# Kernel optimization log

Hardware: AMD Instinct MI355X
Metric: run time of the kernel (lower is better)

The kernel has to match this reference:

```python
import jax, jax.numpy as jnp
import numpy as np
from jax import lax

B_, L, D, EXPAND, N, R, K = 2, 1024, 1024, 2, 16, 64, 4
ED = EXPAND * D


def setup_inputs() -> dict:
    key = jax.random.key(0)
    ks = jax.random.split(key, 8)
    x = jax.random.normal(ks[0], (B_, L, D), dtype=jnp.float32)
    in_proj_w = jax.random.normal(ks[1], (2 * ED, D), dtype=jnp.float32) * (D ** -0.5)
    in_proj_b = jnp.zeros((2 * ED,), jnp.float32)
    conv_w = jax.random.normal(ks[2], (ED, 1, K), dtype=jnp.float32) * (K ** -0.5)
    conv_b = jnp.zeros((ED,), jnp.float32)
    x_proj_w = jax.random.normal(ks[3], (R + 2 * N, ED), dtype=jnp.float32) * (ED ** -0.5)
    dt_proj_w = jax.random.uniform(ks[4], (ED, R), jnp.float32, -(R ** -0.5), R ** -0.5)
    # inverse-softplus of dt ~ U[log(dt_min), log(dt_max)] (matches torch init)
    dt = jnp.exp(jax.random.uniform(ks[5], (ED,), jnp.float32) * (np.log(0.1) - np.log(0.001)) + np.log(0.001))
    dt_proj_b = dt + jnp.log(-jnp.expm1(-dt))  # softplus^{-1}(dt)
    A_log = jnp.log(jnp.broadcast_to(jnp.arange(1, N + 1, dtype=jnp.float32), (ED, N)))
    D_param = jnp.ones((ED,), jnp.float32)
    out_proj_w = jax.random.normal(ks[6], (D, ED), dtype=jnp.float32) * (ED ** -0.5)
    return {"x": x, "in_proj_w": in_proj_w, "in_proj_b": in_proj_b, "conv_w": conv_w,
            "conv_b": conv_b, "x_proj_w": x_proj_w, "dt_proj_w": dt_proj_w,
            "dt_proj_b": dt_proj_b, "A_log": A_log, "D_param": D_param,
            "out_proj_w": out_proj_w}


def _mamba_fwd(x, in_proj_w, in_proj_b, conv_w, conv_b, x_proj_w, dt_proj_w,
               dt_proj_b, A_log, D_param, out_proj_w):
    xz = x @ in_proj_w.T + in_proj_b                       # (B, L, 2*ED)
    xc, z = jnp.split(xz, 2, axis=-1)                      # (B, L, ED) each
    # causal depthwise conv over time (pad left K-1, valid)
    xc = xc.transpose(0, 2, 1)                             # (B, ED, L)
    xc = lax.conv_general_dilated(xc, conv_w, window_strides=(1,),
                                  padding=[(K - 1, 0)], feature_group_count=ED)
    xc = xc + conv_b[None, :, None]
    xc = jax.nn.silu(xc.transpose(0, 2, 1))                # (B, L, ED)
    # SSM params
    A = -jnp.exp(A_log)                                    # (ED, N)
    dbc = xc @ x_proj_w.T                                  # (B, L, R+2N)
    dt, Bmat, Cmat = jnp.split(dbc, [R, R + N], axis=-1)
    dt = jax.nn.softplus(dt @ dt_proj_w.T + dt_proj_b)     # (B, L, ED)
    dA = jnp.exp(dt[..., None] * A)                        # (B, L, ED, N)
    dBx = (dt * xc)[..., None] * Bmat[:, :, None, :]       # (B, L, ED, N)
    # parallel scan: h_t = dA_t * h_{t-1} + dBx_t
    def combine(e1, e2):
        a1, b1 = e1
        a2, b2 = e2
        return a1 * a2, a2 * b1 + b2
    _, hs = lax.associative_scan(combine, (dA, dBx), axis=1)  # (B, L, ED, N)
    y = jnp.einsum('bln,blen->ble', Cmat, hs) + D_param * xc  # (B, L, ED)
    out = (y * jax.nn.silu(z)) @ out_proj_w.T                 # (B, L, D)
    return out


def reference(x, in_proj_w, in_proj_b, conv_w, conv_b, x_proj_w, dt_proj_w,
              dt_proj_b, A_log, D_param, out_proj_w):
    return _mamba_fwd(x, in_proj_w, in_proj_b, conv_w, conv_b, x_proj_w,
                      dt_proj_w, dt_proj_b, A_log, D_param, out_proj_w)
```

## Files before the change

### kernel.cpp

```cpp
#include <hip/hip_runtime.h>
#include <cstddef>


#define BL   2048
#define DIM  1024
#define ED   2048
#define NST  16
#define RLOW 64
#define CH   64
#define LC   16
#define SK   16
#define DBCN 196608

typedef __attribute__((ext_vector_type(4))) float   f32x4;
typedef __attribute__((ext_vector_type(8))) __bf16  bf16x8;
typedef __attribute__((ext_vector_type(8))) unsigned short us8;

__device__ __forceinline__ float silu_(float x) {
  return x / (1.f + __expf(-x));
}

__device__ __forceinline__ float softplus_(float x) {
  const float v = __logf(1.f + __expf(x));
  return (x > 20.f) ? x : v;
}

__device__ __forceinline__ unsigned short f2b(float x) {
  union { float f; unsigned int u; } v; v.f = x;
  unsigned int r = v.u + 0x7FFFu + ((v.u >> 16) & 1u);
  return (unsigned short)(r >> 16);
}

__device__ __forceinline__ float b2f(unsigned short u) {
  union { unsigned int i; float f; } v; v.i = (unsigned int)u << 16; return v.f;
}

__device__ __forceinline__ f32x4 mfma_bf16(us8 a, us8 b, f32x4 c) {
  return __builtin_amdgcn_mfma_f32_16x16x32_bf16(
      __builtin_bit_cast(bf16x8, a), __builtin_bit_cast(bf16x8, b), c, 0, 0, 0);
}

template <int N> __device__ __forceinline__ void vwaitN() {
  if constexpr (N == 0)      asm volatile("s_waitcnt vmcnt(0)" ::: "memory");
  else if constexpr (N == 3) asm volatile("s_waitcnt vmcnt(3)" ::: "memory");
  else if constexpr (N == 4) asm volatile("s_waitcnt vmcnt(4)" ::: "memory");
  else if constexpr (N == 6) asm volatile("s_waitcnt vmcnt(6)" ::: "memory");
  else if constexpr (N == 8) asm volatile("s_waitcnt vmcnt(8)" ::: "memory");
}

#define GLOAD_LDS16(gaddr, laddr)                                              \
  __builtin_amdgcn_global_load_lds(                                            \
      (const __attribute__((address_space(1))) unsigned int*)(gaddr),          \
      (__attribute__((address_space(3))) unsigned int*)(laddr), 16, 0, 0)

template <int BM, int BN, int ACT, bool OBF, int SWZ>
__global__ __launch_bounds__(256) void gemm_bf16(
    const unsigned short* __restrict__ A,
    const unsigned short* __restrict__ W,
    const float* __restrict__ bias,
    void* __restrict__ Cp, int ldc, int Nout, int Kloop, int lda, int sstride)
{
  constexpr int BK     = 32;
  constexpr int FM     = BM / 32;
  constexpr int FN     = BN / 32;
  constexpr int NLA    = BM / 64;
  constexpr int NLW    = BN / 64;
  constexpr int VPS    = NLA + NLW;
  constexpr int ABYTES = BM * BK * 2;
  constexpr int WBYTES = BN * BK * 2;
  __shared__ char smem[4 * (ABYTES + WBYTES)];

  const int tid  = threadIdx.x;
  const int w    = tid >> 6;
  const int lane = tid & 63;
  const int wr   = w >> 1, wc = w & 1;

  int bx = blockIdx.x, by = blockIdx.y;
  if (SWZ) {
    const int nwg  = gridDim.x * gridDim.y;
    const int flat = by * gridDim.x + bx;
    const int nid  = (flat & 7) * (nwg >> 3) + (flat >> 3);
    bx = nid % gridDim.x;
    by = nid / gridDim.x;
  }
  const int bm   = bx * BM;
  const int bn   = by * BN;
  const int kb   = blockIdx.z * Kloop;

  f32x4 acc[FM][FN];
#pragma unroll
  for (int m = 0; m < FM; ++m)
#pragma unroll
    for (int n = 0; n < FN; ++n) acc[m][n] = (f32x4){0.f, 0.f, 0.f, 0.f};

  const int srow = (w << 4) | (lane & 15);
  const int kch  = lane >> 4;
  const int wofs = w * 1024;

  const unsigned short* Ag = A + (size_t)(bm + srow) * lda + kb + kch * 8;
  const unsigned short* Wg = W + (size_t)(bn + srow) * lda + kb + kch * 8;

#define STAGE(cur, k0)                                                         \
  {                                                                            \
    char* ab = smem + (cur) * (ABYTES + WBYTES);                               \
    char* wb = ab + ABYTES;                                                    \
    _Pragma("unroll")                                                          \
    for (int j = 0; j < NLA; ++j)                                              \
      GLOAD_LDS16(Ag + (size_t)(j * 64) * lda + (k0), ab + j * 4096 + wofs);   \
    _Pragma("unroll")                                                          \
    for (int j = 0; j < NLW; ++j)                                              \
      GLOAD_LDS16(Wg + (size_t)(j * 64) * lda + (k0), wb + j * 4096 + wofs);   \
  }

  const int NT = Kloop / BK;
  STAGE(0, 0);
  if (NT > 1) STAGE(1, BK);
  if (NT > 2) STAGE(2, 2 * BK);

  for (int t = 0; t < NT; ++t) {
    if (t <= NT - 3)      vwaitN<2 * VPS>();
    else if (t == NT - 2) vwaitN<VPS>();
    else                  vwaitN<0>();
    __builtin_amdgcn_sched_barrier(0);
    __builtin_amdgcn_s_barrier();
    __builtin_amdgcn_sched_barrier(0);
    if (t + 3 < NT) STAGE((t + 3) & 3, (size_t)(t + 3) * BK);

    const char* ab = smem + (t & 3) * (ABYTES + WBYTES);
    const char* wb = ab + ABYTES;
    us8 af[FM], wf[FN];
#pragma unroll
    for (int m = 0; m < FM; ++m)
      af[m] = *(const us8*)(ab + (wr * FM + m) * 1024 + lane * 16);
#pragma unroll
    for (int n = 0; n < FN; ++n)
      wf[n] = *(const us8*)(wb + (wc * FN + n) * 1024 + lane * 16);
#pragma unroll
    for (int m = 0; m < FM; ++m)
#pragma unroll
      for (int n = 0; n < FN; ++n)
        acc[m][n] = mfma_bf16(af[m], wf[n], acc[m][n]);
  }
#undef STAGE

  const int rbase = (lane >> 4) * 4;
  float* Cf = (float*)Cp + (size_t)blockIdx.z * sstride;
#pragma unroll
  for (int m = 0; m < FM; ++m) {
#pragma unroll
    for (int n = 0; n < FN; ++n) {
      const int col = bn + wc * (BN / 2) + n * 16 + (lane & 15);
      if (col < Nout) {
        const float bv = bias ? bias[col] : 0.f;
#pragma unroll
        for (int r = 0; r < 4; ++r) {
          const int row = bm + wr * (BM / 2) + m * 16 + rbase + r;
          float v = acc[m][n][r] + bv;
          if (ACT == 1) v = softplus_(v);
          if (OBF) ((unsigned short*)Cp)[(size_t)row * ldc + col] = f2b(v);
          else     Cf[(size_t)row * ldc + col] = v;
        }
      }
    }
  }
}

__global__ __launch_bounds__(256) void reduce_dbc_k(
    const float* __restrict__ par, float* __restrict__ dbc,
    unsigned short* __restrict__ dtA)
{
  const int i = blockIdx.x * 256 + threadIdx.x;
  float4 s = ((const float4*)par)[i];
#pragma unroll
  for (int sk = 1; sk < SK; ++sk) {
    float4 v = ((const float4*)(par + (size_t)sk * DBCN))[i];
    s.x += v.x; s.y += v.y; s.z += v.z; s.w += v.w;
  }
  ((float4*)dbc)[i] = s;
  const int row = i / 24, c4 = i % 24;
  if (c4 < 16) {
    ushort4 o;
    o.x = f2b(s.x); o.y = f2b(s.y); o.z = f2b(s.z); o.w = f2b(s.w);
    ((ushort4*)(dtA + (size_t)row * 64))[c4] = o;
  }
}

__global__ __launch_bounds__(256) void reduce_out_k(
    const float* __restrict__ par, float* __restrict__ out)
{
  const int i = blockIdx.x * 256 + threadIdx.x;
  float4 a = ((const float4*)par)[i];
#pragma unroll
  for (int k = 1; k < 4; ++k) {
    float4 b = ((const float4*)(par + (size_t)k * 2097152))[i];
    a.x += b.x; a.y += b.y; a.z += b.z; a.w += b.w;
  }
  ((float4*)out)[i] = a;
}

__global__ __launch_bounds__(256) void cvt_all_k(
    const float* __restrict__ x, const float* __restrict__ inw,
    const float* __restrict__ ow, const float* __restrict__ xpw,
    const float* __restrict__ dtw,
    unsigned short* __restrict__ xb, unsigned short* __restrict__ iwb,
    unsigned short* __restrict__ owb, unsigned short* __restrict__ xpwb,
    unsigned short* __restrict__ dtwb)
{
  const int i = blockIdx.x * 256 + threadIdx.x;
  const float* src; unsigned short* dst; int j;
  if (i < 524288)       { src = x;   dst = xb;  j = i; }
  else if (i < 1572864) { src = inw; dst = iwb; j = i - 524288; }
  else if (i < 2097152) { src = ow;  dst = owb; j = i - 1572864; }
  else if (i < 2162688) {
    j = i - 2097152;
    const int idx = j * 4;
    ushort4 o = {0, 0, 0, 0};
    if ((idx >> 11) < 96) {
      float4 v = *(const float4*)(xpw + idx);
      o.x = f2b(v.x); o.y = f2b(v.y); o.z = f2b(v.z); o.w = f2b(v.w);
    }
    *(ushort4*)(xpwb + idx) = o;
    return;
  } else                { src = dtw; dst = dtwb; j = i - 2162688; }
  float4 v = ((const float4*)src)[j];
  ushort4 o;
  o.x = f2b(v.x); o.y = f2b(v.y); o.z = f2b(v.z); o.w = f2b(v.w);
  ((ushort4*)dst)[j] = o;
}

__global__ __launch_bounds__(256) void conv_silu_k(
    const unsigned short* __restrict__ xzb, const float* __restrict__ cw,
    const float* __restrict__ cb, unsigned short* __restrict__ xcb)
{
  const int idx = blockIdx.x * 256 + threadIdx.x;
  const int row = idx >> 9;
  const int e   = (idx & 511) * 4;
  const int l   = row & 1023;
  const unsigned short* base = xzb + (size_t)(row - l) * (2 * ED) + e;

  float4 cbv = *(const float4*)(cb + e);
  float a0 = cbv.x, a1 = cbv.y, a2 = cbv.z, a3 = cbv.w;
#pragma unroll
  for (int k = 0; k < 4; ++k) {
    const int ls = l - 3 + k;
    if (ls >= 0) {
      ushort4 u = *(const ushort4*)(base + (size_t)ls * (2 * ED));
      a0 += cw[(size_t)(e + 0) * 4 + k] * b2f(u.x);
      a1 += cw[(size_t)(e + 1) * 4 + k] * b2f(u.y);
      a2 += cw[(size_t)(e + 2) * 4 + k] * b2f(u.z);
      a3 += cw[(size_t)(e + 3) * 4 + k] * b2f(u.w);
    }
  }
  ushort4 o;
  o.x = f2b(silu_(a0)); o.y = f2b(silu_(a1));
  o.z = f2b(silu_(a2)); o.w = f2b(silu_(a3));
  *(ushort4*)(xcb + (size_t)row * ED + e) = o;
}

__global__ __launch_bounds__(256, 4) void scan_phase1(
    const unsigned short* __restrict__ dt, const unsigned short* __restrict__ xcb,
    const float* __restrict__ dbc, const float* __restrict__ A_log,
    float* __restrict__ aprod_o, float* __restrict__ bfin_o)
{
  const int g  = blockIdx.x * 256 + threadIdx.x;
  const int e  = g & (ED - 1);
  const int bc = g >> 11;
  const int b  = bc >> 6;
  const int c  = bc & (CH - 1);
  const size_t rowbase = (size_t)b * 1024 + (size_t)c * LC;

  __shared__ float4 sB[LC][4];
  if (threadIdx.x < LC * 4) {
    const int row = threadIdx.x >> 2, q = threadIdx.x & 3;
    sB[row][q] = ((const float4*)(dbc + (rowbase + row) * 96 + RLOW))[q];
  }
  __syncthreads();

  float Aen[NST];
  {
    const float4* Ap = (const float4*)(A_log + (size_t)e * NST);
#pragma unroll
    for (int q = 0; q < 4; ++q) {
      float4 v = Ap[q];
      Aen[q*4+0] = -__expf(v.x); Aen[q*4+1] = -__expf(v.y);
      Aen[q*4+2] = -__expf(v.z); Aen[q*4+3] = -__expf(v.w);
    }
  }

  float dtv[LC], dxv[LC];
#pragma unroll
  for (int i = 0; i < LC; ++i) dtv[i] = b2f(dt[(rowbase + i) * ED + e]);
#pragma unroll
  for (int i = 0; i < LC; ++i)
    dxv[i] = dtv[i] * b2f(xcb[(rowbase + i) * ED + e]);

  float h[NST], ap[NST];
#pragma unroll
  for (int n = 0; n < NST; ++n) { h[n] = 0.f; ap[n] = 1.f; }

  for (int i = 0; i < LC; ++i) {
    float Bv[NST];
#pragma unroll
    for (int q = 0; q < 4; ++q) {
      float4 v = sB[i][q];
      Bv[q*4+0]=v.x; Bv[q*4+1]=v.y; Bv[q*4+2]=v.z; Bv[q*4+3]=v.w;
    }
#pragma unroll
    for (int n = 0; n < NST; ++n) {
      const float dA = __expf(dtv[i] * Aen[n]);
      ap[n] *= dA;
      h[n] = fmaf(dA, h[n], dxv[i] * Bv[n]);
    }
  }

  const size_t obase = ((size_t)(b * ED + e) * CH + c) * NST;
  float4* ao = (float4*)(aprod_o + obase);
  float4* bo = (float4*)(bfin_o + obase);
#pragma unroll
  for (int q = 0; q < 4; ++q) {
    ao[q] = make_float4(ap[q*4+0], ap[q*4+1], ap[q*4+2], ap[q*4+3]);
    bo[q] = make_float4(h[q*4+0],  h[q*4+1],  h[q*4+2],  h[q*4+3]);
  }
}

__global__ __launch_bounds__(256) void scan_phase2(
    const float* __restrict__ aprod, float* __restrict__ bfin)
{
  const int be   = blockIdx.x * 4 + (threadIdx.x >> 6);
  const int lane = threadIdx.x & 63;
  const size_t base = (size_t)be * CH * NST;

  float Aa[NST], Bb[NST];
  {
    const float4* ap4 = (const float4*)(aprod + base);
    const float4* bp4 = (const float4*)(bfin + base);
#pragma unroll
    for (int q = 0; q < 4; ++q) {
      float4 v = ap4[lane * 4 + q];
      Aa[q*4+0]=v.x; Aa[q*4+1]=v.y; Aa[q*4+2]=v.z; Aa[q*4+3]=v.w;
      float4 w = bp4[lane * 4 + q];
      Bb[q*4+0]=w.x; Bb[q*4+1]=w.y; Bb[q*4+2]=w.z; Bb[q*4+3]=w.w;
    }
  }

#pragma unroll
  for (int d = 1; d < 64; d <<= 1) {
#pragma unroll
    for (int r = 0; r < NST; ++r) {
      const float aP = __shfl_up(Aa[r], d);
      const float bP = __shfl_up(Bb[r], d);
      if (lane >= d) {
        Bb[r] = fmaf(Aa[r], bP, Bb[r]);
        Aa[r] *= aP;
      }
    }
  }

#pragma unroll
  for (int r = 0; r < NST; ++r) {
    const float hs = __shfl_up(Bb[r], 1);
    Bb[r] = (lane == 0) ? 0.f : hs;
  }

  float4* ob4 = (float4*)(bfin + base);
#pragma unroll
  for (int q = 0; q < 4; ++q)
    ob4[lane * 4 + q] = make_float4(Bb[q*4+0], Bb[q*4+1], Bb[q*4+2], Bb[q*4+3]);
}

__global__ __launch_bounds__(256, 4) void scan_phase3(
    const unsigned short* __restrict__ dt, const unsigned short* __restrict__ xcb,
    const float* __restrict__ dbc, const float* __restrict__ A_log,
    const float* __restrict__ Dp, const unsigned short* __restrict__ xzb,
    const float* __restrict__ hst, unsigned short* __restrict__ ygb)
{
  const int g  = blockIdx.x * 256 + threadIdx.x;
  const int e  = g & (ED - 1);
  const int bc = g >> 11;
  const int b  = bc >> 6;
  const int c  = bc & (CH - 1);
  const size_t rowbase = (size_t)b * 1024 + (size_t)c * LC;

  __shared__ float4 sBC[LC][8];
  if (threadIdx.x < LC * 8) {
    const int row = threadIdx.x >> 3, q = threadIdx.x & 7;
    sBC[row][q] = ((const float4*)(dbc + (rowbase + row) * 96 + RLOW))[q];
  }
  __syncthreads();

  float Aen[NST];
  {
    const float4* Ap = (const float4*)(A_log + (size_t)e * NST);
#pragma unroll
    for (int q = 0; q < 4; ++q) {
      float4 v = Ap[q];
      Aen[q*4+0] = -__expf(v.x); Aen[q*4+1] = -__expf(v.y);
      Aen[q*4+2] = -__expf(v.z); Aen[q*4+3] = -__expf(v.w);
    }
  }

  float dtv[LC], xcv[LC];
#pragma unroll
  for (int i = 0; i < LC; ++i) dtv[i] = b2f(dt[(rowbase + i) * ED + e]);
#pragma unroll
  for (int i = 0; i < LC; ++i) xcv[i] = b2f(xcb[(rowbase + i) * ED + e]);

  float h[NST];
  {
    const float4* Hp = (const float4*)(hst + ((size_t)(b * ED + e) * CH + c) * NST);
#pragma unroll
    for (int q = 0; q < 4; ++q) {
      float4 v = Hp[q];
      h[q*4+0]=v.x; h[q*4+1]=v.y; h[q*4+2]=v.z; h[q*4+3]=v.w;
    }
  }

  const float De = Dp[e];
  for (int i = 0; i < LC; ++i) {
    const size_t rr = rowbase + i;
    float Bv[NST], Cv[NST];
#pragma unroll
    for (int q = 0; q < 4; ++q) {
      float4 v = sBC[i][q];
      Bv[q*4+0]=v.x; Bv[q*4+1]=v.y; Bv[q*4+2]=v.z; Bv[q*4+3]=v.w;
      float4 w = sBC[i][q + 4];
      Cv[q*4+0]=w.x; Cv[q*4+1]=w.y; Cv[q*4+2]=w.z; Cv[q*4+3]=w.w;
    }
    const float dx = dtv[i] * xcv[i];
    float y = 0.f;
#pragma unroll
    for (int n = 0; n < NST; ++n) {
      const float dA = __expf(dtv[i] * Aen[n]);
      h[n] = fmaf(dA, h[n], dx * Bv[n]);
      y = fmaf(Cv[n], h[n], y);
    }
    y = fmaf(De, xcv[i], y);
    const float zf = b2f(xzb[rr * (2 * ED) + ED + e]);
    ygb[rr * ED + e] = f2b(y * silu_(zf));
  }
}

extern "C" void kernel_launch(void* const* d_in, const int* in_sizes, int n_in,
                              void* d_out, int out_size, void* d_ws, size_t ws_size,
                              hipStream_t stream) {
  const float* x         = (const float*)d_in[0];
  const float* in_w      = (const float*)d_in[1];
  const float* in_b      = (const float*)d_in[2];
  const float* conv_w    = (const float*)d_in[3];
  const float* conv_b    = (const float*)d_in[4];
  const float* xproj_w   = (const float*)d_in[5];
  const float* dtproj_w  = (const float*)d_in[6];
  const float* dtproj_b  = (const float*)d_in[7];
  const float* A_log     = (const float*)d_in[8];
  const float* D_param   = (const float*)d_in[9];
  const float* outproj_w = (const float*)d_in[10];
  float* out = (float*)d_out;

  float* ws    = (float*)d_ws;
  float* dbc   = ws;
  unsigned short* dtbu = (unsigned short*)(dbc + 196608);
  float* aprod = (float*)(dtbu + 4194304);
  float* bfin  = aprod + 4194304;
  float* parx  = bfin  + 4194304;
  unsigned short* xzb  = (unsigned short*)(parx + 3145728);
  unsigned short* xb   = xzb  + 8388608;
  unsigned short* iwb  = xb   + 2097152;
  unsigned short* owb  = iwb  + 4194304;
  unsigned short* xpwb = owb  + 2097152;
  unsigned short* xcb  = xpwb + 262144;
  unsigned short* ygb  = xcb  + 4194304;
  unsigned short* dtA  = ygb  + 4194304;
  unsigned short* dtwb = dtA  + 131072;
  float* paro  = aprod;

  const dim3 blk(256);

  cvt_all_k<<<dim3(2195456 / 256), blk, 0, stream>>>(
      x, in_w, outproj_w, xproj_w, dtproj_w, xb, iwb, owb, xpwb, dtwb);

  gemm_bf16<128, 128, 0, true, 1><<<dim3(BL / 128, 4096 / 128), blk, 0, stream>>>(
      xb, iwb, in_b, xzb, 2 * ED, 2 * ED, DIM, DIM, 0);

  conv_silu_k<<<dim3((BL * (ED / 4)) / 256), blk, 0, stream>>>(
      xzb, conv_w, conv_b, xcb);

  gemm_bf16<128, 128, 0, false, 0><<<dim3(BL / 128, 1, SK), blk, 0, stream>>>(
      xcb, xpwb, nullptr, parx, 96, 96, ED / SK, ED, DBCN);
  reduce_dbc_k<<<dim3(DBCN / 4 / 256), blk, 0, stream>>>(parx, dbc, dtA);

  gemm_bf16<64, 128, 1, true, 0><<<dim3(BL / 64, ED / 128), blk, 0, stream>>>(
      dtA, dtwb, dtproj_b, dtbu, ED, ED, RLOW, RLOW, 0);

  scan_phase1<<<dim3((2 * CH * ED) / 256), blk, 0, stream>>>(
      dtbu, xcb, dbc, A_log, aprod, bfin);
  scan_phase2<<<dim3((2 * ED) / 4), blk, 0, stream>>>(aprod, bfin);
  scan_phase3<<<dim3((2 * CH * ED) / 256), blk, 0, stream>>>(
      dtbu, xcb, dbc, A_log, D_param, xzb, bfin, ygb);

  gemm_bf16<128, 128, 0, false, 0><<<dim3(BL / 128, 1024 / 128, 4), blk, 0, stream>>>(
      ygb, owb, nullptr, paro, DIM, DIM, ED / 4, ED, 2097152);
  reduce_out_k<<<dim3(2097152 / 4 / 256), blk, 0, stream>>>(paro, out);
}
```

Baseline: 191.7 us.

## Give each wave private LDS double buffers and drop block barriers in GEMM

The bf16 GEMM now has each wave load its own A and W sub-tiles into a private double-buffered LDS region instead of sharing a four-stage block-wide buffer. This removes the per-iteration s_barrier, since no wave reads data loaded by another wave. The cost is duplicated global loads, because waves sharing a row or column of the tile each fetch the same data. Prefetch depth also drops from three stages to one, which may expose more memory latency.

```diff
diff --git a/kernel.cpp b/kernel.cpp
--- a/kernel.cpp
+++ b/kernel.cpp
@@ -42,8 +42,6 @@
 
 template <int N> __device__ __forceinline__ void vwaitN() {
   if constexpr (N == 0)      asm volatile("s_waitcnt vmcnt(0)" ::: "memory");
-  else if constexpr (N == 3) asm volatile("s_waitcnt vmcnt(3)" ::: "memory");
-  else if constexpr (N == 4) asm volatile("s_waitcnt vmcnt(4)" ::: "memory");
   else if constexpr (N == 6) asm volatile("s_waitcnt vmcnt(6)" ::: "memory");
   else if constexpr (N == 8) asm volatile("s_waitcnt vmcnt(8)" ::: "memory");
 }
@@ -60,15 +58,14 @@
     const float* __restrict__ bias,
     void* __restrict__ Cp, int ldc, int Nout, int Kloop, int lda, int sstride)
 {
-  constexpr int BK     = 32;
-  constexpr int FM     = BM / 32;
-  constexpr int FN     = BN / 32;
-  constexpr int NLA    = BM / 64;
-  constexpr int NLW    = BN / 64;
-  constexpr int VPS    = NLA + NLW;
-  constexpr int ABYTES = BM * BK * 2;
-  constexpr int WBYTES = BN * BK * 2;
-  __shared__ char smem[4 * (ABYTES + WBYTES)];
+  constexpr int BK  = 32;
+  constexpr int WM  = BM / 2, WN = BN / 2;
+  constexpr int FMW = WM / 16, FNW = WN / 16;
+  constexpr int VPS = FMW + FNW;
+  constexpr int AB  = WM * BK * 2;
+  constexpr int WBb = WN * BK * 2;
+  constexpr int BUF = AB + WBb;
+  __shared__ char smem[4 * 2 * BUF];
 
   const int tid  = threadIdx.x;
   const int w    = tid >> 6;
@@ -83,62 +80,58 @@
     bx = nid % gridDim.x;
     by = nid / gridDim.x;
   }
-  const int bm   = bx * BM;
-  const int bn   = by * BN;
-  const int kb   = blockIdx.z * Kloop;
-
-  f32x4 acc[FM][FN];
-#pragma unroll
-  for (int m = 0; m < FM; ++m)
-#pragma unroll
-    for (int n = 0; n < FN; ++n) acc[m][n] = (f32x4){0.f, 0.f, 0.f, 0.f};
-
-  const int srow = (w << 4) | (lane & 15);
-  const int kch  = lane >> 4;
-  const int wofs = w * 1024;
-
-  const unsigned short* Ag = A + (size_t)(bm + srow) * lda + kb + kch * 8;
-  const unsigned short* Wg = W + (size_t)(bn + srow) * lda + kb + kch * 8;
-
-#define STAGE(cur, k0)                                                         \
+  const int bm = bx * BM;
+  const int bn = by * BN;
+  const int kb = blockIdx.z * Kloop;
+
+  f32x4 acc[FMW][FNW];
+#pragma unroll
+  for (int m = 0; m < FMW; ++m)
+#pragma unroll
+    for (int n = 0; n < FNW; ++n) acc[m][n] = (f32x4){0.f, 0.f, 0.f, 0.f};
+
+  char* wbase = smem + w * 2 * BUF;
+  const unsigned short* Ag =
+      A + (size_t)(bm + wr * WM + (lane & 15)) * lda + kb + (lane >> 4) * 8;
+  const unsigned short* Wg =
+      W + (size_t)(bn + wc * WN + (lane & 15)) * lda + kb + (lane >> 4) * 8;
+
+#define STAGE(bb, k0)                                                          \
   {                                                                            \
-    char* ab = smem + (cur) * (ABYTES + WBYTES);                               \
-    char* wb = ab + ABYTES;                                                    \
+    char* dst = wbase + (bb) * BUF;                                            \
     _Pragma("unroll")                                                          \
-    for (int j = 0; j < NLA; ++j)                                              \
-      GLOAD_LDS16(Ag + (size_t)(j * 64) * lda + (k0), ab + j * 4096 + wofs);   \
+    for (int j = 0; j < FMW; ++j)                                              \
+      GLOAD_LDS16(Ag + (size_t)(j * 16) * lda + (k0), dst + j * 1024);         \
     _Pragma("unroll")                                                          \
-    for (int j = 0; j < NLW; ++j)                                              \
-      GLOAD_LDS16(Wg + (size_t)(j * 64) * lda + (k0), wb + j * 4096 + wofs);   \
+    for (int j = 0; j < FNW; ++j)                                              \
+      GLOAD_LDS16(Wg + (size_t)(j * 16) * lda + (k0), dst + AB + j * 1024);    \
   }
 
   const int NT = Kloop / BK;
   STAGE(0, 0);
   if (NT > 1) STAGE(1, BK);
-  if (NT > 2) STAGE(2, 2 * BK);
 
   for (int t = 0; t < NT; ++t) {
-    if (t <= NT - 3)      vwaitN<2 * VPS>();
-    else if (t == NT - 2) vwaitN<VPS>();
-    else                  vwaitN<0>();
+    if (t + 1 < NT) vwaitN<VPS>();
+    else            vwaitN<0>();
     __builtin_amdgcn_sched_barrier(0);
-    __builtin_amdgcn_s_barrier();
+
+    const char* bufc = wbase + (t & 1) * BUF;
+    us8 af[FMW], wf[FNW];
+#pragma unroll
+    for (int m = 0; m < FMW; ++m)
+      af[m] = *(const us8*)(bufc + m * 1024 + lane * 16);
+#pragma unroll
+    for (int n = 0; n < FNW; ++n)
+      wf[n] = *(const us8*)(bufc + AB + n * 1024 + lane * 16);
+    asm volatile("s_waitcnt lgkmcnt(0)" ::: "memory");
     __builtin_amdgcn_sched_barrier(0);
-    if (t + 3 < NT) STAGE((t + 3) & 3, (size_t)(t + 3) * BK);
-
-    const char* ab = smem + (t & 3) * (ABYTES + WBYTES);
-    const char* wb = ab + ABYTES;
-    us8 af[FM], wf[FN];
-#pragma unroll
-    for (int m = 0; m < FM; ++m)
-      af[m] = *(const us8*)(ab + (wr * FM + m) * 1024 + lane * 16);
-#pragma unroll
-    for (int n = 0; n < FN; ++n)
-      wf[n] = *(const us8*)(wb + (wc * FN + n) * 1024 + lane * 16);
-#pragma unroll
-    for (int m = 0; m < FM; ++m)
-#pragma unroll
-      for (int n = 0; n < FN; ++n)
+    if (t + 2 < NT) STAGE(t & 1, (size_t)(t + 2) * BK);
+
+#pragma unroll
+    for (int m = 0; m < FMW; ++m)
+#pragma unroll
+      for (int n = 0; n < FNW; ++n)
         acc[m][n] = mfma_bf16(af[m], wf[n], acc[m][n]);
   }
 #undef STAGE
@@ -146,15 +139,15 @@
   const int rbase = (lane >> 4) * 4;
   float* Cf = (float*)Cp + (size_t)blockIdx.z * sstride;
 #pragma unroll
-  for (int m = 0; m < FM; ++m) {
-#pragma unroll
-    for (int n = 0; n < FN; ++n) {
-      const int col = bn + wc * (BN / 2) + n * 16 + (lane & 15);
+  for (int m = 0; m < FMW; ++m) {
+#pragma unroll
+    for (int n = 0; n < FNW; ++n) {
+      const int col = bn + wc * WN + n * 16 + (lane & 15);
       if (col < Nout) {
         const float bv = bias ? bias[col] : 0.f;
 #pragma unroll
         for (int r = 0; r < 4; ++r) {
-          const int row = bm + wr * (BM / 2) + m * 16 + rbase + r;
+          const int row = bm + wr * WM + m * 16 + rbase + r;
           float v = acc[m][n][r] + bv;
           if (ACT == 1) v = softplus_(v);
           if (OBF) ((unsigned short*)Cp)[(size_t)row * ldc + col] = f2b(v);
```

Result: slower. 233.0 us (+21.5%).
